# Kernel tuning notes

Measured on AMD Instinct MI355X. Metric: run time of the kernel, lower is better.

## Reference

```python
import jax, jax.numpy as jnp
import numpy as np

B, N, D_IN, D_OUT = 16, 512, 256, 32
C_SP, H, W = 64, 256, 256


def setup_inputs() -> dict:
    key = jax.random.key(0)
    k1, k2, k3, k4, k5 = jax.random.split(key, 5)
    return {
        "spatial_info": jax.random.normal(k1, (B, C_SP, H, W), dtype=jnp.float32),
        "entity_embeddings": jax.random.normal(k2, (B, N, D_IN), dtype=jnp.float32),
        "W_proj": jax.random.normal(k3, (D_IN, D_OUT), dtype=jnp.float32) / np.sqrt(D_IN),
        "b_proj": jax.random.normal(k4, (D_OUT,), dtype=jnp.float32) * 0.01,
        "locations": jax.random.randint(k5, (B, N, 2), 0, 256, dtype=jnp.int32),
    }


def reference(spatial_info, entity_embeddings, W_proj, b_proj, locations):
    # per-entity linear projection (fc_block): [B, N, D_out]
    proj = jnp.einsum('bnd,de->bne', entity_embeddings, W_proj) + b_proj

    Bb, C, Hh, Ww = spatial_info.shape
    # clamp locations like the torch min/max logic
    h = jnp.clip(locations[..., 0], 0, Hh - 1)  # [B, N]
    w = jnp.clip(locations[..., 1], 0, Ww - 1)  # [B, N]
    flat = h * Ww + w                            # [B, N] flattened spatial index

    scatter_map = jnp.zeros((Bb, Hh * Ww, proj.shape[-1]), dtype=spatial_info.dtype)
    b_idx = jnp.arange(Bb, dtype=flat.dtype)[:, None]  # [B, 1]
    scatter_map = scatter_map.at[b_idx, flat].set(proj)
    scatter_map = scatter_map.reshape(Bb, Hh, Ww, -1).transpose(0, 3, 1, 2)  # [B, D_out, H, W]

    return jnp.concatenate([spatial_info, scatter_map], axis=1)
```

## Files before the change

kernel.cpp:

```cpp
#include <hip/hip_runtime.h>

#define BATCH 16
#define NENT  512
#define D_IN  256
#define D_OUT 32
#define CSP   64
#define COUT  96
#define HWDIM 256
#define HWSZ  65536
#define HW4   16384
#define SP_B4  (CSP * HW4)
#define SC_B4  (D_OUT * HW4)
#define OUT_B4 (COUT * HW4)

__global__ void zero_kernel(float4* __restrict__ out,
                            int4* __restrict__ owner4) {
    const int SC_TOT = BATCH * SC_B4;
    const int OW4    = BATCH * HWSZ / 4;
    const int total  = SC_TOT + OW4;
    const int stride = gridDim.x * blockDim.x;
    const float4 z4 = make_float4(0.f, 0.f, 0.f, 0.f);
    for (int i = blockIdx.x * blockDim.x + threadIdx.x; i < total; i += stride) {
        if (i < SC_TOT) {
            int b = i >> 19;
            int r = i & (SC_B4 - 1);
            out[(size_t)b * OUT_B4 + SP_B4 + r] = z4;
        } else {
            owner4[i - SC_TOT] = make_int4(0, 0, 0, 0);
        }
    }
}

__global__ void owner_kernel(const int* __restrict__ loc,
                             int* __restrict__ owner) {
    int gid = blockIdx.x * blockDim.x + threadIdx.x;
    if (gid >= BATCH * NENT) return;
    int h = loc[gid * 2 + 0];
    int w = loc[gid * 2 + 1];
    h = min(max(h, 0), HWDIM - 1);
    w = min(max(w, 0), HWDIM - 1);
    int b = gid >> 9;
    int n = gid & (NENT - 1);
    atomicMax(&owner[b * HWSZ + h * HWDIM + w], n + 1);
}

__global__ void copy_kernel(const float4* __restrict__ sp,
                            float4* __restrict__ out) {
    const int PER = 2048 * 256;
    int b = blockIdx.y;
    int t = blockIdx.x * blockDim.x + threadIdx.x;
    const float4* spb  = sp  + (size_t)b * SP_B4;
    float4*       outb = out + (size_t)b * OUT_B4;
    outb[t]       = spb[t];
    outb[t + PER] = spb[t + PER];
}

__global__ void proj_scatter_kernel(const float* __restrict__ emb,
                                    const float* __restrict__ Wp,
                                    const float* __restrict__ bp,
                                    const int* __restrict__ loc,
                                    const int* __restrict__ owner,
                                    float* __restrict__ out) {
    int gid = blockIdx.x * blockDim.x + threadIdx.x;
    int ent = gid >> 5;
    int e   = gid & 31;
    int b   = ent >> 9;
    int n   = ent & (NENT - 1);

    int h = loc[ent * 2 + 0];
    int w = loc[ent * 2 + 1];
    h = min(max(h, 0), HWDIM - 1);
    w = min(max(w, 0), HWDIM - 1);
    int flat = h * HWDIM + w;

    if (owner[b * HWSZ + flat] != n + 1) return;

    float acc = bp[e];
    const float* er = emb + ent * D_IN;
    #pragma unroll 8
    for (int d = 0; d < D_IN; ++d) {
        acc += er[d] * Wp[d * D_OUT + e];
    }
    out[(size_t)b * (COUT * HWSZ) + (CSP + e) * HWSZ + flat] = acc;
}

extern "C" void kernel_launch(void* const* d_in, const int* in_sizes, int n_in,
                              void* d_out, int out_size, void* d_ws, size_t ws_size,
                              hipStream_t stream) {
    const float* spatial = (const float*)d_in[0];
    const float* emb     = (const float*)d_in[1];
    const float* Wp      = (const float*)d_in[2];
    const float* bp      = (const float*)d_in[3];
    const int*   loc     = (const int*)d_in[4];
    float* out = (float*)d_out;
    int* owner = (int*)d_ws;

    zero_kernel<<<2048, 256, 0, stream>>>((float4*)out, (int4*)owner);
    owner_kernel<<<32, 256, 0, stream>>>(loc, owner);
    dim3 cgrid(2048, BATCH);
    copy_kernel<<<cgrid, 256, 0, stream>>>((const float4*)spatial, (float4*)out);
    proj_scatter_kernel<<<1024, 256, 0, stream>>>(emb, Wp, bp, loc, owner, out);
}
```

Measured before the change: 165.2 us.

## Fold scatter-region zeroing into copy pass and clear only touched owner cells

```diff
diff --git a/kernel.cpp b/kernel.cpp
--- a/kernel.cpp
+++ b/kernel.cpp
@@ -13,46 +13,37 @@
 #define SC_B4  (D_OUT * HW4)
 #define OUT_B4 (COUT * HW4)
 
-__global__ void zero_kernel(float4* __restrict__ out,
-                            int4* __restrict__ owner4) {
-    const int SC_TOT = BATCH * SC_B4;
-    const int OW4    = BATCH * HWSZ / 4;
-    const int total  = SC_TOT + OW4;
-    const int stride = gridDim.x * blockDim.x;
-    const float4 z4 = make_float4(0.f, 0.f, 0.f, 0.f);
-    for (int i = blockIdx.x * blockDim.x + threadIdx.x; i < total; i += stride) {
-        if (i < SC_TOT) {
-            int b = i >> 19;
-            int r = i & (SC_B4 - 1);
-            out[(size_t)b * OUT_B4 + SP_B4 + r] = z4;
-        } else {
-            owner4[i - SC_TOT] = make_int4(0, 0, 0, 0);
-        }
-    }
+__global__ void zero_cells_kernel(const int* __restrict__ loc,
+                                  int* __restrict__ owner) {
+    int gid = blockIdx.x * blockDim.x + threadIdx.x;
+    if (gid >= BATCH * NENT) return;
+    int h = min(max(loc[gid * 2 + 0], 0), HWDIM - 1);
+    int w = min(max(loc[gid * 2 + 1], 0), HWDIM - 1);
+    int b = gid >> 9;
+    owner[b * HWSZ + h * HWDIM + w] = 0;
 }
 
 __global__ void owner_kernel(const int* __restrict__ loc,
                              int* __restrict__ owner) {
     int gid = blockIdx.x * blockDim.x + threadIdx.x;
     if (gid >= BATCH * NENT) return;
-    int h = loc[gid * 2 + 0];
-    int w = loc[gid * 2 + 1];
-    h = min(max(h, 0), HWDIM - 1);
-    w = min(max(w, 0), HWDIM - 1);
+    int h = min(max(loc[gid * 2 + 0], 0), HWDIM - 1);
+    int w = min(max(loc[gid * 2 + 1], 0), HWDIM - 1);
     int b = gid >> 9;
     int n = gid & (NENT - 1);
     atomicMax(&owner[b * HWSZ + h * HWDIM + w], n + 1);
 }
 
-__global__ void copy_kernel(const float4* __restrict__ sp,
-                            float4* __restrict__ out) {
+__global__ void bigpass_kernel(const float4* __restrict__ sp,
+                               float4* __restrict__ out) {
     const int PER = 2048 * 256;
     int b = blockIdx.y;
     int t = blockIdx.x * blockDim.x + threadIdx.x;
     const float4* spb  = sp  + (size_t)b * SP_B4;
     float4*       outb = out + (size_t)b * OUT_B4;
-    outb[t]       = spb[t];
-    outb[t + PER] = spb[t + PER];
+    outb[t]            = spb[t];
+    outb[t + PER]      = spb[t + PER];
+    outb[SP_B4 + t]    = make_float4(0.f, 0.f, 0.f, 0.f);
 }
 
 __global__ void proj_scatter_kernel(const float* __restrict__ emb,
@@ -67,19 +58,22 @@
     int b   = ent >> 9;
     int n   = ent & (NENT - 1);
 
-    int h = loc[ent * 2 + 0];
-    int w = loc[ent * 2 + 1];
-    h = min(max(h, 0), HWDIM - 1);
-    w = min(max(w, 0), HWDIM - 1);
+    int h = min(max(loc[ent * 2 + 0], 0), HWDIM - 1);
+    int w = min(max(loc[ent * 2 + 1], 0), HWDIM - 1);
     int flat = h * HWDIM + w;
 
     if (owner[b * HWSZ + flat] != n + 1) return;
 
+    const float4* er4 = (const float4*)(emb + (size_t)ent * D_IN);
     float acc = bp[e];
-    const float* er = emb + ent * D_IN;
     #pragma unroll 8
-    for (int d = 0; d < D_IN; ++d) {
-        acc += er[d] * Wp[d * D_OUT + e];
+    for (int d4 = 0; d4 < D_IN / 4; ++d4) {
+        float4 ev = er4[d4];
+        int d = d4 * 4;
+        acc += ev.x * Wp[(d + 0) * D_OUT + e];
+        acc += ev.y * Wp[(d + 1) * D_OUT + e];
+        acc += ev.z * Wp[(d + 2) * D_OUT + e];
+        acc += ev.w * Wp[(d + 3) * D_OUT + e];
     }
     out[(size_t)b * (COUT * HWSZ) + (CSP + e) * HWSZ + flat] = acc;
 }
@@ -95,9 +89,10 @@
     float* out = (float*)d_out;
     int* owner = (int*)d_ws;
 
-    zero_kernel<<<2048, 256, 0, stream>>>((float4*)out, (int4*)owner);
+    zero_cells_kernel<<<32, 256, 0, stream>>>(loc, owner);
     owner_kernel<<<32, 256, 0, stream>>>(loc, owner);
-    dim3 cgrid(2048, BATCH);
-    copy_kernel<<<cgrid, 256, 0, stream>>>((const float4*)spatial, (float4*)out);
+    dim3 grid(2048, BATCH);
+    bigpass_kernel<<<grid, 256, 0, stream>>>((const float4*)spatial,
+                                             (float4*)out);
     proj_scatter_kernel<<<1024, 256, 0, stream>>>(emb, Wp, bp, loc, owner, out);
 }
```

Result: slower. 170.5 us (+3.2%).
